# Kernel optimization log

Measured on AMD Instinct MI355X. Metric: run time of the kernel, lower is better.

The kernel has to match this reference:

```python
import jax, jax.numpy as jnp
import numpy as np

N_NODES = 100000
N_EDGES = 3200000
D_IN = 32
N_HEADS = 4
D_HEAD = 8  # N_HEADS * D_HEAD == D_IN so residual connection is valid


def setup_inputs() -> dict:
    key = jax.random.key(0)
    k1, k2, k3, k4, k5, k6, k7 = jax.random.split(key, 7)
    scale = 1.0 / np.sqrt(D_IN)
    x = jax.random.normal(k1, (N_NODES, D_IN), dtype=jnp.float32)
    Wq = jax.random.normal(k2, (D_IN, N_HEADS * D_HEAD), dtype=jnp.float32) * scale
    Wk = jax.random.normal(k3, (D_IN, N_HEADS * D_HEAD), dtype=jnp.float32) * scale
    Wv = jax.random.normal(k4, (D_IN, N_HEADS * D_HEAD), dtype=jnp.float32) * scale
    Wo = jax.random.normal(k5, (N_HEADS * D_HEAD, D_IN), dtype=jnp.float32) * scale
    src = jax.random.randint(k6, (N_EDGES,), 0, N_NODES)
    dst = jax.random.randint(k7, (N_EDGES,), 0, N_NODES)
    edge_index = jnp.stack([src, dst], axis=0).astype(jnp.int64)
    return {"x": x, "Wq": Wq, "Wk": Wk, "Wv": Wv, "Wo": Wo, "edge_index": edge_index}


def reference(x, Wq, Wk, Wv, Wo, edge_index):
    # Graph-transformer attention message passing over an edge list:
    # gather (q at dst, k/v at src) -> per-edge scores -> segment softmax over
    # incoming edges of each destination node -> scatter-sum weighted values.
    N = x.shape[0]
    src, dst = edge_index[0], edge_index[1]
    q = (x @ Wq).reshape(N, N_HEADS, D_HEAD)
    k = (x @ Wk).reshape(N, N_HEADS, D_HEAD)
    v = (x @ Wv).reshape(N, N_HEADS, D_HEAD)
    inv_sqrt_d = jnp.asarray(1.0 / np.sqrt(D_HEAD), dtype=x.dtype)
    # per-edge attention logits: [E, H]
    scores = jnp.einsum('ehd,ehd->eh', q[dst], k[src]) * inv_sqrt_d
    # numerically stable segment softmax over edges grouped by dst
    m = jax.ops.segment_max(scores, dst, num_segments=N)  # [N, H]
    m = jnp.where(jnp.isfinite(m), m, jnp.zeros_like(m))  # nodes with no in-edges
    e = jnp.exp(scores - m[dst])                           # [E, H]
    denom = jax.ops.segment_sum(e, dst, num_segments=N)    # [N, H]
    msg = jax.ops.segment_sum(e[:, :, None] * v[src], dst, num_segments=N)  # [N, H, Dh]
    attn_out = msg / jnp.maximum(denom, 1e-16)[:, :, None]
    out = attn_out.reshape(N, N_HEADS * D_HEAD) @ Wo
    return x + out  # residual
```

## Files before the change

### kernel.cpp

```cpp
#include <hip/hip_runtime.h>
#include <hip/hip_fp16.h>
#include <math.h>

#define D_IN 32
#define NH 4
#define DH 8

#define BUCKET_BITS 7
#define BUCKET_N    128
#define CAP         4608
#define PCHUNK      4096
#define NBK_MAX     1024

typedef __attribute__((ext_vector_type(8))) _Float16 half8;
typedef __attribute__((ext_vector_type(2))) _Float16 half2v;

__device__ __forceinline__ float fdot8v(half8 a, half8 b) {
    half2v a0 = {a[0], a[1]}, a1 = {a[2], a[3]}, a2 = {a[4], a[5]}, a3 = {a[6], a[7]};
    half2v b0 = {b[0], b[1]}, b1 = {b[2], b[3]}, b2 = {b[4], b[5]}, b3 = {b[6], b[7]};
    float acc = 0.f;
    acc = __builtin_amdgcn_fdot2(a0, b0, acc, false);
    acc = __builtin_amdgcn_fdot2(a1, b1, acc, false);
    acc = __builtin_amdgcn_fdot2(a2, b2, acc, false);
    acc = __builtin_amdgcn_fdot2(a3, b3, acc, false);
    return acc;
}

__global__ void qkv_kernel(const float* __restrict__ x,
                           const float* __restrict__ Wq,
                           const float* __restrict__ Wk,
                           const float* __restrict__ Wv,
                           _Float16* __restrict__ qh,
                           _Float16* __restrict__ kv,
                           int* __restrict__ gcur,
                           int N) {
    if (blockIdx.x == 0) {
        for (int i = threadIdx.x; i < NBK_MAX; i += blockDim.x) gcur[i] = 0;
    }
    __shared__ float sWq[1024], sWk[1024], sWv[1024];
    for (int i = threadIdx.x; i < 1024; i += blockDim.x) {
        sWq[i] = Wq[i];
        sWk[i] = Wk[i];
        sWv[i] = Wv[i];
    }
    __syncthreads();
    int n = blockIdx.x * blockDim.x + threadIdx.x;
    if (n >= N) return;

    float xr[32];
    const float4* x4 = (const float4*)(x + (size_t)n * 32);
    #pragma unroll
    for (int i = 0; i < 8; i++) {
        float4 f = x4[i];
        xr[4*i+0] = f.x; xr[4*i+1] = f.y; xr[4*i+2] = f.z; xr[4*i+3] = f.w;
    }

    const float scale = 0.35355339059327373f * 1.4426950408889634f;
    float acc[32];

    #pragma unroll
    for (int j = 0; j < 32; j++) acc[j] = 0.f;
    for (int i = 0; i < 32; i++) {
        float xi = xr[i];
        #pragma unroll
        for (int j = 0; j < 32; j++) acc[j] += xi * sWq[i*32 + j];
    }
    {
        _Float16* o = qh + ((size_t)n << 5);
        #pragma unroll
        for (int i = 0; i < 4; i++) {
            half8 hv;
            #pragma unroll
            for (int j = 0; j < 8; j++) hv[j] = (_Float16)(acc[i*8 + j] * scale);
            *(half8*)(o + i*8) = hv;
        }
    }

    #pragma unroll
    for (int j = 0; j < 32; j++) acc[j] = 0.f;
    for (int i = 0; i < 32; i++) {
        float xi = xr[i];
        #pragma unroll
        for (int j = 0; j < 32; j++) acc[j] += xi * sWk[i*32 + j];
    }
    {
        _Float16* o = kv + ((size_t)n << 6);
        #pragma unroll
        for (int i = 0; i < 4; i++) {
            half8 hv;
            #pragma unroll
            for (int j = 0; j < 8; j++) hv[j] = (_Float16)acc[i*8 + j];
            *(half8*)(o + i*8) = hv;
        }
    }

    #pragma unroll
    for (int j = 0; j < 32; j++) acc[j] = 0.f;
    for (int i = 0; i < 32; i++) {
        float xi = xr[i];
        #pragma unroll
        for (int j = 0; j < 32; j++) acc[j] += xi * sWv[i*32 + j];
    }
    {
        _Float16* o = kv + ((size_t)n << 6) + 32;
        #pragma unroll
        for (int i = 0; i < 4; i++) {
            half8 hv;
            #pragma unroll
            for (int j = 0; j < 8; j++) hv[j] = (_Float16)acc[i*8 + j];
            *(half8*)(o + i*8) = hv;
        }
    }
}

__global__ __launch_bounds__(512) void bucketize_kernel(const int* __restrict__ src,
                                                        const int* __restrict__ dst,
                                                        int* __restrict__ gcur,
                                                        unsigned* __restrict__ packed,
                                                        int E, int nbuckets) {
    __shared__ int hcnt[NBK_MAX];
    __shared__ int loff[NBK_MAX];
    __shared__ int hbase[NBK_MAX];
    __shared__ unsigned sbuf[PCHUNK];
    __shared__ unsigned short sbkt[PCHUNK];

    int t = threadIdx.x;
    for (int i = t; i < NBK_MAX; i += 512) hcnt[i] = 0;
    __syncthreads();

    int b0 = blockIdx.x * PCHUNK;
    int end = min(b0 + PCHUNK, E);

    unsigned pval[8];
    int      pbr[8];
    #pragma unroll
    for (int j = 0; j < 8; j++) {
        int e = b0 + t + j * 512;
        if (e < end) {
            int d = dst[e];
            int bkt = d >> BUCKET_BITS;
            int r = atomicAdd(&hcnt[bkt], 1);
            pval[j] = (unsigned)src[e] | ((unsigned)(d & (BUCKET_N - 1)) << 17);
            pbr[j]  = (bkt << 16) | r;
        }
    }
    __syncthreads();

    for (int i = t; i < NBK_MAX; i += 512) {
        int c = hcnt[i];
        if (c > 0 && i < nbuckets) hbase[i] = atomicAdd(&gcur[i], c);
    }
    if (t < 64) {
        int sums[16]; int tot = 0;
        #pragma unroll
        for (int j = 0; j < 16; j++) { sums[j] = hcnt[t*16 + j]; tot += sums[j]; }
        int incl = tot;
        #pragma unroll
        for (int o = 1; o < 64; o <<= 1) {
            int u = __shfl_up(incl, o);
            if (t >= o) incl += u;
        }
        int run = incl - tot;
        #pragma unroll
        for (int j = 0; j < 16; j++) { loff[t*16 + j] = run; run += sums[j]; }
    }
    __syncthreads();

    #pragma unroll
    for (int j = 0; j < 8; j++) {
        int e = b0 + t + j * 512;
        if (e < end) {
            int bkt = pbr[j] >> 16;
            int r   = pbr[j] & 0xFFFF;
            int pos = loff[bkt] + r;
            sbuf[pos] = pval[j];
            sbkt[pos] = (unsigned short)bkt;
        }
    }
    __syncthreads();

    int cnt = end - b0;
    for (int i = t; i < cnt; i += 512) {
        int bkt = sbkt[i];
        int gpos = hbase[bkt] + (i - loff[bkt]);
        if (gpos < CAP)
            packed[(size_t)bkt * CAP + gpos] = sbuf[i];
    }
}

__global__ __launch_bounds__(512) void fused_kernel(const _Float16* __restrict__ qh,
                                                    const _Float16* __restrict__ kv,
                                                    const unsigned* __restrict__ packed,
                                                    const int* __restrict__ gcur,
                                                    const float* __restrict__ x,
                                                    const float* __restrict__ Wo,
                                                    float* __restrict__ out,
                                                    int N) {
    __shared__ float sWo[1024];
    __shared__ int hist[BUCKET_N];
    __shared__ int soff[BUCKET_N + 1];
    __shared__ int eLDS[CAP];
    __shared__ float sAttn[8][2][32];

    int b = blockIdx.x;
    int t = threadIdx.x;

    for (int i = t; i < 1024; i += 512) sWo[i] = Wo[i];
    if (t < BUCKET_N) hist[t] = 0;
    __syncthreads();

    int cnt = min(gcur[b], CAP);
    size_t base = (size_t)b * CAP;

    unsigned pv[9];
    int      pr[9];
    #pragma unroll
    for (int j = 0; j < 9; j++) {
        int i = t + j * 512;
        if (i < cnt) {
            unsigned p = packed[base + i];
            int ld = p >> 17;
            int r = atomicAdd(&hist[ld], 1);
            pv[j] = p;
            pr[j] = (ld << 16) | r;
        }
    }
    __syncthreads();

    if (t < 64) {
        int s0 = hist[2*t], s1 = hist[2*t + 1];
        int tot = s0 + s1;
        int incl = tot;
        #pragma unroll
        for (int o = 1; o < 64; o <<= 1) {
            int u = __shfl_up(incl, o);
            if (t >= o) incl += u;
        }
        int run = incl - tot;
        soff[2*t]     = run;
        soff[2*t + 1] = run + s0;
        if (t == 63) soff[BUCKET_N] = run + tot;
    }
    __syncthreads();

    #pragma unroll
    for (int j = 0; j < 9; j++) {
        int i = t + j * 512;
        if (i < cnt) {
            int ld = pr[j] >> 16;
            int r  = pr[j] & 0xFFFF;
            eLDS[soff[ld] + r] = (int)(pv[j] & 0x1FFFFu);
        }
    }
    __syncthreads();

    int wid  = t >> 6;
    int lane = t & 63;
    int nh   = lane >> 5;
    int l5   = lane & 31;
    int h    = l5 & 3;
    int slot = l5 >> 2;
    int node0 = b << BUCKET_BITS;

    for (int widx = wid * 2 + nh; widx < BUCKET_N; widx += 16) {
        int n = node0 + widx;
        bool valid = n < N;

        float d = 0.f;
        float msg[8];
        #pragma unroll
        for (int j = 0; j < 8; j++) msg[j] = 0.f;

        if (valid) {
            int e0 = soff[widx];
            int e1 = soff[widx + 1];

            half8 qa = *(const half8*)(qh + ((size_t)n << 5) + (h << 3));

            for (int bb = e0; bb < e1; bb += 16) {
                int ea = bb + slot;
                int eb = ea + 8;
                int ca = min(ea, e1 - 1);
                int cb = min(eb, e1 - 1);
                int sa = eLDS[ca];
                int sb = eLDS[cb];
                const _Float16* ra = kv + ((size_t)sa << 6) + (h << 3);
                const _Float16* rb = kv + ((size_t)sb << 6) + (h << 3);
                half8 ka = *(const half8*)ra;
                half8 va = *(const half8*)(ra + 32);
                half8 kb = *(const half8*)rb;
                half8 vb = *(const half8*)(rb + 32);
                float wA = (ea < e1) ? exp2f(fdot8v(qa, ka)) : 0.f;
                float wB = (eb < e1) ? exp2f(fdot8v(qa, kb)) : 0.f;
                d += wA + wB;
                #pragma unroll
                for (int j = 0; j < 8; j++)
                    msg[j] += wA * (float)va[j] + wB * (float)vb[j];
            }
        }

        #pragma unroll
        for (int mask = 4; mask < 32; mask <<= 1) {
            d += __shfl_xor(d, mask);
            #pragma unroll
            for (int j = 0; j < 8; j++) msg[j] += __shfl_xor(msg[j], mask);
        }

        if (valid && slot == 0) {
            float inv = 1.0f / fmaxf(d, 1e-16f);
            #pragma unroll
            for (int j = 0; j < 8; j++) sAttn[wid][nh][h * 8 + j] = msg[j] * inv;
        }

        if (valid) {
            int col = l5;
            float acc = x[(size_t)n * 32 + col];
            #pragma unroll
            for (int i = 0; i < 32; i++)
                acc += sAttn[wid][nh][i] * sWo[i * 32 + col];
            out[(size_t)n * 32 + col] = acc;
        }
    }
}

extern "C" void kernel_launch(void* const* d_in, const int* in_sizes, int n_in,
                              void* d_out, int out_size, void* d_ws, size_t ws_size,
                              hipStream_t stream) {
    const float* x  = (const float*)d_in[0];
    const float* Wq = (const float*)d_in[1];
    const float* Wk = (const float*)d_in[2];
    const float* Wv = (const float*)d_in[3];
    const float* Wo = (const float*)d_in[4];
    const int*   ei = (const int*)d_in[5];

    const int N = in_sizes[0] / D_IN;
    const int E = in_sizes[5] / 2;
    const int* src = ei;
    const int* dst = ei + E;

    const int nbuckets = (N + BUCKET_N - 1) >> BUCKET_BITS;

    _Float16* qh     = (_Float16*)d_ws;
    _Float16* kv     = qh + (size_t)N * 32;
    int*      gcur   = (int*)(kv + (size_t)N * 64);
    unsigned* packed = (unsigned*)(gcur + NBK_MAX);

    qkv_kernel<<<(N + 255) / 256, 256, 0, stream>>>(x, Wq, Wk, Wv, qh, kv, gcur, N);

    bucketize_kernel<<<(E + PCHUNK - 1) / PCHUNK, 512, 0, stream>>>(
        src, dst, gcur, packed, E, nbuckets);

    fused_kernel<<<nbuckets, 512, 0, stream>>>(qh, kv, packed, gcur, x, Wo,
                                               (float*)d_out, N);
}
```

Baseline: 125.5 us.

## Merge QKV projection and edge bucketization into one heterogeneous prep kernel

Combines the QKV projection kernel and the edge bucketize kernel into a single launch. The first blocks bucketize edge chunks and the remaining blocks compute the QKV projections, with both sharing one raw shared-memory buffer. Zeroing of the bucket counters moves to a hipMemsetAsync, since the old in-kernel zeroing would now race with blocks doing the atomic adds. The aim is to remove a launch and the serialization between two independent stages so they overlap on the GPU. In exchange it adds a memset node, uses a larger shared-memory footprint for the QKV blocks, and moves QKV to 512-thread blocks.

```diff
diff --git a/kernel.cpp b/kernel.cpp
--- a/kernel.cpp
+++ b/kernel.cpp
@@ -26,165 +26,166 @@
     return acc;
 }
 
-__global__ void qkv_kernel(const float* __restrict__ x,
-                           const float* __restrict__ Wq,
-                           const float* __restrict__ Wk,
-                           const float* __restrict__ Wv,
-                           _Float16* __restrict__ qh,
-                           _Float16* __restrict__ kv,
-                           int* __restrict__ gcur,
-                           int N) {
-    if (blockIdx.x == 0) {
-        for (int i = threadIdx.x; i < NBK_MAX; i += blockDim.x) gcur[i] = 0;
-    }
-    __shared__ float sWq[1024], sWk[1024], sWv[1024];
-    for (int i = threadIdx.x; i < 1024; i += blockDim.x) {
-        sWq[i] = Wq[i];
-        sWk[i] = Wk[i];
-        sWv[i] = Wv[i];
-    }
-    __syncthreads();
-    int n = blockIdx.x * blockDim.x + threadIdx.x;
-    if (n >= N) return;
-
-    float xr[32];
-    const float4* x4 = (const float4*)(x + (size_t)n * 32);
-    #pragma unroll
-    for (int i = 0; i < 8; i++) {
-        float4 f = x4[i];
-        xr[4*i+0] = f.x; xr[4*i+1] = f.y; xr[4*i+2] = f.z; xr[4*i+3] = f.w;
-    }
-
-    const float scale = 0.35355339059327373f * 1.4426950408889634f;
-    float acc[32];
-
-    #pragma unroll
-    for (int j = 0; j < 32; j++) acc[j] = 0.f;
-    for (int i = 0; i < 32; i++) {
-        float xi = xr[i];
-        #pragma unroll
-        for (int j = 0; j < 32; j++) acc[j] += xi * sWq[i*32 + j];
-    }
-    {
-        _Float16* o = qh + ((size_t)n << 5);
-        #pragma unroll
-        for (int i = 0; i < 4; i++) {
-            half8 hv;
-            #pragma unroll
-            for (int j = 0; j < 8; j++) hv[j] = (_Float16)(acc[i*8 + j] * scale);
-            *(half8*)(o + i*8) = hv;
-        }
-    }
-
-    #pragma unroll
-    for (int j = 0; j < 32; j++) acc[j] = 0.f;
-    for (int i = 0; i < 32; i++) {
-        float xi = xr[i];
-        #pragma unroll
-        for (int j = 0; j < 32; j++) acc[j] += xi * sWk[i*32 + j];
-    }
-    {
-        _Float16* o = kv + ((size_t)n << 6);
-        #pragma unroll
-        for (int i = 0; i < 4; i++) {
-            half8 hv;
-            #pragma unroll
-            for (int j = 0; j < 8; j++) hv[j] = (_Float16)acc[i*8 + j];
-            *(half8*)(o + i*8) = hv;
-        }
-    }
-
-    #pragma unroll
-    for (int j = 0; j < 32; j++) acc[j] = 0.f;
-    for (int i = 0; i < 32; i++) {
-        float xi = xr[i];
-        #pragma unroll
-        for (int j = 0; j < 32; j++) acc[j] += xi * sWv[i*32 + j];
-    }
-    {
-        _Float16* o = kv + ((size_t)n << 6) + 32;
-        #pragma unroll
-        for (int i = 0; i < 4; i++) {
-            half8 hv;
-            #pragma unroll
-            for (int j = 0; j < 8; j++) hv[j] = (_Float16)acc[i*8 + j];
-            *(half8*)(o + i*8) = hv;
-        }
-    }
-}
-
-__global__ __launch_bounds__(512) void bucketize_kernel(const int* __restrict__ src,
-                                                        const int* __restrict__ dst,
-                                                        int* __restrict__ gcur,
-                                                        unsigned* __restrict__ packed,
-                                                        int E, int nbuckets) {
-    __shared__ int hcnt[NBK_MAX];
-    __shared__ int loff[NBK_MAX];
-    __shared__ int hbase[NBK_MAX];
-    __shared__ unsigned sbuf[PCHUNK];
-    __shared__ unsigned short sbkt[PCHUNK];
-
+__global__ __launch_bounds__(512) void prep_kernel(const float* __restrict__ x,
+                                                   const float* __restrict__ Wq,
+                                                   const float* __restrict__ Wk,
+                                                   const float* __restrict__ Wv,
+                                                   _Float16* __restrict__ qh,
+                                                   _Float16* __restrict__ kv,
+                                                   const int* __restrict__ src,
+                                                   const int* __restrict__ dst,
+                                                   int* __restrict__ gcur,
+                                                   unsigned* __restrict__ packed,
+                                                   int E, int N,
+                                                   int nbuckets, int nchunks) {
+    __shared__ __align__(16) unsigned char smem[36864];
     int t = threadIdx.x;
-    for (int i = t; i < NBK_MAX; i += 512) hcnt[i] = 0;
-    __syncthreads();
-
-    int b0 = blockIdx.x * PCHUNK;
-    int end = min(b0 + PCHUNK, E);
-
-    unsigned pval[8];
-    int      pbr[8];
-    #pragma unroll
-    for (int j = 0; j < 8; j++) {
-        int e = b0 + t + j * 512;
-        if (e < end) {
-            int d = dst[e];
-            int bkt = d >> BUCKET_BITS;
-            int r = atomicAdd(&hcnt[bkt], 1);
-            pval[j] = (unsigned)src[e] | ((unsigned)(d & (BUCKET_N - 1)) << 17);
-            pbr[j]  = (bkt << 16) | r;
-        }
-    }
-    __syncthreads();
-
-    for (int i = t; i < NBK_MAX; i += 512) {
-        int c = hcnt[i];
-        if (c > 0 && i < nbuckets) hbase[i] = atomicAdd(&gcur[i], c);
-    }
-    if (t < 64) {
-        int sums[16]; int tot = 0;
-        #pragma unroll
-        for (int j = 0; j < 16; j++) { sums[j] = hcnt[t*16 + j]; tot += sums[j]; }
-        int incl = tot;
-        #pragma unroll
-        for (int o = 1; o < 64; o <<= 1) {
-            int u = __shfl_up(incl, o);
-            if (t >= o) incl += u;
-        }
-        int run = incl - tot;
-        #pragma unroll
-        for (int j = 0; j < 16; j++) { loff[t*16 + j] = run; run += sums[j]; }
-    }
-    __syncthreads();
-
-    #pragma unroll
-    for (int j = 0; j < 8; j++) {
-        int e = b0 + t + j * 512;
-        if (e < end) {
-            int bkt = pbr[j] >> 16;
-            int r   = pbr[j] & 0xFFFF;
-            int pos = loff[bkt] + r;
-            sbuf[pos] = pval[j];
-            sbkt[pos] = (unsigned short)bkt;
-        }
-    }
-    __syncthreads();
-
-    int cnt = end - b0;
-    for (int i = t; i < cnt; i += 512) {
-        int bkt = sbkt[i];
-        int gpos = hbase[bkt] + (i - loff[bkt]);
-        if (gpos < CAP)
-            packed[(size_t)bkt * CAP + gpos] = sbuf[i];
+
+    if (blockIdx.x < (unsigned)nchunks) {
+        int* hcnt  = (int*)smem;
+        int* loff  = hcnt + NBK_MAX;
+        int* hbase = loff + NBK_MAX;
+        unsigned* sbuf = (unsigned*)(hbase + NBK_MAX);
+        unsigned short* sbkt = (unsigned short*)(sbuf + PCHUNK);
+
+        for (int i = t; i < NBK_MAX; i += 512) hcnt[i] = 0;
+        __syncthreads();
+
+        int b0 = blockIdx.x * PCHUNK;
+        int end = min(b0 + PCHUNK, E);
+
+        unsigned pval[8];
+        int      pbr[8];
+        #pragma unroll
+        for (int j = 0; j < 8; j++) {
+            int e = b0 + t + j * 512;
+            if (e < end) {
+                int d = dst[e];
+                int bkt = d >> BUCKET_BITS;
+                int r = atomicAdd(&hcnt[bkt], 1);
+                pval[j] = (unsigned)src[e] | ((unsigned)(d & (BUCKET_N - 1)) << 17);
+                pbr[j]  = (bkt << 16) | r;
+            }
+        }
+        __syncthreads();
+
+        for (int i = t; i < NBK_MAX; i += 512) {
+            int c = hcnt[i];
+            if (c > 0 && i < nbuckets) hbase[i] = atomicAdd(&gcur[i], c);
+        }
+        if (t < 64) {
+            int sums[16]; int tot = 0;
+            #pragma unroll
+            for (int j = 0; j < 16; j++) { sums[j] = hcnt[t*16 + j]; tot += sums[j]; }
+            int incl = tot;
+            #pragma unroll
+            for (int o = 1; o < 64; o <<= 1) {
+                int u = __shfl_up(incl, o);
+                if (t >= o) incl += u;
+            }
+            int run = incl - tot;
+            #pragma unroll
+            for (int j = 0; j < 16; j++) { loff[t*16 + j] = run; run += sums[j]; }
+        }
+        __syncthreads();
+
+        #pragma unroll
+        for (int j = 0; j < 8; j++) {
+            int e = b0 + t + j * 512;
+            if (e < end) {
+                int bkt = pbr[j] >> 16;
+                int r   = pbr[j] & 0xFFFF;
+                int pos = loff[bkt] + r;
+                sbuf[pos] = pval[j];
+                sbkt[pos] = (unsigned short)bkt;
+            }
+        }
+        __syncthreads();
+
+        int cnt = end - b0;
+        for (int i = t; i < cnt; i += 512) {
+            int bkt = sbkt[i];
+            int gpos = hbase[bkt] + (i - loff[bkt]);
+            if (gpos < CAP)
+                packed[(size_t)bkt * CAP + gpos] = sbuf[i];
+        }
+    } else {
+        float* sWq = (float*)smem;
+        float* sWk = sWq + 1024;
+        float* sWv = sWk + 1024;
+        for (int i = t; i < 1024; i += 512) {
+            sWq[i] = Wq[i];
+            sWk[i] = Wk[i];
+            sWv[i] = Wv[i];
+        }
+        __syncthreads();
+        int n = (blockIdx.x - nchunks) * 512 + t;
+        if (n >= N) return;
+
+        float xr[32];
+        const float4* x4 = (const float4*)(x + (size_t)n * 32);
+        #pragma unroll
+        for (int i = 0; i < 8; i++) {
+            float4 f = x4[i];
+            xr[4*i+0] = f.x; xr[4*i+1] = f.y; xr[4*i+2] = f.z; xr[4*i+3] = f.w;
+        }
+
+        const float scale = 0.35355339059327373f * 1.4426950408889634f;
+        float acc[32];
+
+        #pragma unroll
+        for (int j = 0; j < 32; j++) acc[j] = 0.f;
+        for (int i = 0; i < 32; i++) {
+            float xi = xr[i];
+            #pragma unroll
+            for (int j = 0; j < 32; j++) acc[j] += xi * sWq[i*32 + j];
+        }
+        {
+            _Float16* o = qh + ((size_t)n << 5);
+            #pragma unroll
+            for (int i = 0; i < 4; i++) {
+                half8 hv;
+                #pragma unroll
+                for (int j = 0; j < 8; j++) hv[j] = (_Float16)(acc[i*8 + j] * scale);
+                *(half8*)(o + i*8) = hv;
+            }
+        }
+
+        #pragma unroll
+        for (int j = 0; j < 32; j++) acc[j] = 0.f;
+        for (int i = 0; i < 32; i++) {
+            float xi = xr[i];
+            #pragma unroll
+            for (int j = 0; j < 32; j++) acc[j] += xi * sWk[i*32 + j];
+        }
+        {
+            _Float16* o = kv + ((size_t)n << 6);
+            #pragma unroll
+            for (int i = 0; i < 4; i++) {
+                half8 hv;
+                #pragma unroll
+                for (int j = 0; j < 8; j++) hv[j] = (_Float16)acc[i*8 + j];
+                *(half8*)(o + i*8) = hv;
+            }
+        }
+
+        #pragma unroll
+        for (int j = 0; j < 32; j++) acc[j] = 0.f;
+        for (int i = 0; i < 32; i++) {
+            float xi = xr[i];
+            #pragma unroll
+            for (int j = 0; j < 32; j++) acc[j] += xi * sWv[i*32 + j];
+        }
+        {
+            _Float16* o = kv + ((size_t)n << 6) + 32;
+            #pragma unroll
+            for (int i = 0; i < 4; i++) {
+                half8 hv;
+                #pragma unroll
+                for (int j = 0; j < 8; j++) hv[j] = (_Float16)acc[i*8 + j];
+                *(half8*)(o + i*8) = hv;
+            }
+        }
     }
 }
 
@@ -339,16 +340,19 @@
     const int* dst = ei + E;
 
     const int nbuckets = (N + BUCKET_N - 1) >> BUCKET_BITS;
+    const int nchunks  = (E + PCHUNK - 1) / PCHUNK;
+    const int nqkv     = (N + 511) / 512;
 
     _Float16* qh     = (_Float16*)d_ws;
     _Float16* kv     = qh + (size_t)N * 32;
     int*      gcur   = (int*)(kv + (size_t)N * 64);
     unsigned* packed = (unsigned*)(gcur + NBK_MAX);
 
-    qkv_kernel<<<(N + 255) / 256, 256, 0, stream>>>(x, Wq, Wk, Wv, qh, kv, gcur, N);
-
-    bucketize_kernel<<<(E + PCHUNK - 1) / PCHUNK, 512, 0, stream>>>(
-        src, dst, gcur, packed, E, nbuckets);
+    hipMemsetAsync(gcur, 0, NBK_MAX * sizeof(int), stream);
+
+    prep_kernel<<<nchunks + nqkv, 512, 0, stream>>>(x, Wq, Wk, Wv, qh, kv,
+                                                    src, dst, gcur, packed,
+                                                    E, N, nbuckets, nchunks);
 
     fused_kernel<<<nbuckets, 512, 0, stream>>>(qh, kv, packed, gcur, x, Wo,
                                                (float*)d_out, N);
```

New measurement: 120.6 us. 1.04x faster.
